# Performance work log

Hardware: AMD Instinct MI355X
Metric: run time of the kernel (lower is better)

Reference implementation:

```python
import jax, jax.numpy as jnp
import numpy as np

N = 100_000           # nodes
E = 3_200_000         # edges (avg degree 32)
DIMS = [64, 80, 160, 112, 160, 176, 96, 144, 96, 128, 96, 160]
NUM_CLASSES = 2


def setup_inputs() -> dict:
    key = jax.random.key(0)
    ks = jax.random.split(key, 64)
    inp = {}
    inp['x'] = jax.random.normal(ks[0], (N, DIMS[0]), dtype=jnp.float32)
    inp['src'] = jax.random.randint(ks[1], (E,), 0, N, dtype=jnp.int32)
    inp['dst'] = jax.random.randint(ks[2], (E,), 0, N, dtype=jnp.int32)
    inp['edata'] = jax.random.uniform(ks[3], (E,), dtype=jnp.float32)
    for i in range(11):
        fi, fo = DIMS[i], DIMS[i + 1]
        inp[f'W{i+1}'] = jax.random.normal(ks[4 + i], (fi, fo), dtype=jnp.float32) / np.float32(np.sqrt(fi))
        inp[f'b{i+1}'] = jnp.zeros((fo,), dtype=jnp.float32)
    inp['Wd1'] = jax.random.normal(ks[20], (160, 140), dtype=jnp.float32) / np.float32(np.sqrt(160))
    inp['bd1'] = jnp.zeros((140,), dtype=jnp.float32)
    inp['Wd2'] = jax.random.normal(ks[21], (140, NUM_CLASSES), dtype=jnp.float32) / np.float32(np.sqrt(140))
    inp['bd2'] = jnp.zeros((NUM_CLASSES,), dtype=jnp.float32)
    inp['mu'] = jnp.asarray(0.0, dtype=jnp.float32)
    inp['sigma'] = jnp.asarray(1.0, dtype=jnp.float32)
    return inp


def _forward(x, src, dst, edata, Ws, bs, Wd1, bd1, Wd2, bd2, mu, sigma):
    n = x.shape[0]
    # edge-weight transform: keep w=1 edges, else gaussian kernel; mu/sigma read via .item() -> stop_gradient
    mu_c = jax.lax.stop_gradient(mu)
    sg_c = jax.lax.stop_gradient(sigma)
    w = jnp.where(edata == 1.0, edata, jnp.exp(-((edata - mu_c) ** 2) / sg_c))  # [E]
    ones_e = jnp.ones_like(edata)
    deg_out = jax.ops.segment_sum(ones_e, src, num_segments=n)  # [N]
    deg_in = jax.ops.segment_sum(ones_e, dst, num_segments=n)   # [N]
    ns = jnp.where(deg_out > 0, jax.lax.rsqrt(jnp.maximum(deg_out, 1.0)), 0.0)
    nd = jnp.where(deg_in > 0, jax.lax.rsqrt(jnp.maximum(deg_in, 1.0)), 0.0)
    coef = ns[src] * w  # [E] src-side norm fused with edge weight

    h = x
    for W, b in zip(Ws, bs):
        m = h[src] * coef[:, None]                               # gather + weight  [E, F]
        agg = jax.ops.segment_sum(m, dst, num_segments=n)        # scatter-add      [N, F]
        h = jax.nn.leaky_relu((agg * nd[:, None]) @ W + b)       # norm + linear + act

    h = jax.nn.leaky_relu(jnp.mean(h, axis=0))                   # mean_nodes -> [160]
    h = jax.nn.leaky_relu(h @ Wd1 + bd1)                         # dropout = identity (eval)
    return jax.nn.sigmoid(h @ Wd2 + bd2)                         # [NUM_CLASSES]


def reference(x, src, dst, edata,
              W1, b1, W2, b2, W3, b3, W4, b4, W5, b5, W6, b6,
              W7, b7, W8, b8, W9, b9, W10, b10, W11, b11,
              Wd1, bd1, Wd2, bd2, mu, sigma):
    Ws = [W1, W2, W3, W4, W5, W6, W7, W8, W9, W10, W11]
    bs = [b1, b2, b3, b4, b5, b6, b7, b8, b9, b10, b11]
    return _forward(x, src, dst, edata, Ws, bs, Wd1, bd1, Wd2, bd2, mu, sigma)
```

## Files before the change

kernel.cpp:

```cpp
#include <hip/hip_runtime.h>

#define LEAKY(v) ((v) > 0.0f ? (v) : 0.01f * (v))
#define SCAN_BLK 1024
#define EPB 4096
#define BKN 256

typedef __bf16 bf16x8 __attribute__((ext_vector_type(8)));
typedef float f32x4 __attribute__((ext_vector_type(4)));

__device__ inline float bflo(unsigned int u) { return __uint_as_float(u << 16); }
__device__ inline float bfhi(unsigned int u) { return __uint_as_float(u & 0xFFFF0000u); }
__device__ inline unsigned int pack2bf(float lo, float hi) {
    unsigned int a = __float_as_uint(lo);
    unsigned int b = __float_as_uint(hi);
    a = (a + 0x7FFFu + ((a >> 16) & 1u)) >> 16;
    b = (b + 0x7FFFu + ((b >> 16) & 1u)) & 0xFFFF0000u;
    return a | b;
}
__device__ inline unsigned short f2bf(float f) {
    unsigned int u = __float_as_uint(f);
    return (unsigned short)((u + 0x7FFFu + ((u >> 16) & 1u)) >> 16);
}

__device__ inline unsigned char f2f8(float v) {
    return (unsigned char)(__builtin_amdgcn_cvt_pk_fp8_f32(v, 0.0f, 0u, false) & 0xFFu);
}


__global__ void histo_kernel(const int* __restrict__ src, const int* __restrict__ dst,
                             int* __restrict__ bh, int E, int NBK, int NBLK, int LEN) {
    extern __shared__ int lds[];
    int* hs = lds;
    int* hd = lds + NBK;
    for (int j = threadIdx.x; j < 2 * NBK; j += 512) lds[j] = 0;
    __syncthreads();
    int b = blockIdx.x;
    int e0 = b * EPB, e1 = min(e0 + EPB, E);
    for (int e = e0 + threadIdx.x; e < e1; e += 512) {
        atomicAdd(&hs[src[e] >> 8], 1);
        atomicAdd(&hd[dst[e] >> 8], 1);
    }
    __syncthreads();
    for (int j = threadIdx.x; j < NBK; j += 512) {
        bh[j * NBLK + b] = hs[j];
        bh[LEN + j * NBLK + b] = hd[j];
    }
}

__global__ void scan1_kernel(const int* __restrict__ deg, int* __restrict__ out,
                             int* __restrict__ bsums, int n) {
    __shared__ int sh[SCAN_BLK];
    int gid = blockIdx.x * SCAN_BLK + threadIdx.x;
    int v = (gid < n) ? deg[gid] : 0;
    sh[threadIdx.x] = v;
    __syncthreads();
    for (int off = 1; off < SCAN_BLK; off <<= 1) {
        int t = (threadIdx.x >= off) ? sh[threadIdx.x - off] : 0;
        __syncthreads();
        sh[threadIdx.x] += t;
        __syncthreads();
    }
    if (gid < n) out[gid + 1] = sh[threadIdx.x];
    if (threadIdx.x == SCAN_BLK - 1) bsums[blockIdx.x] = sh[threadIdx.x];
    if (gid == 0) out[0] = 0;
}

__global__ void scan2_kernel(int* __restrict__ bsums, int nb) {
    __shared__ int sh[SCAN_BLK];
    int v = (threadIdx.x < nb) ? bsums[threadIdx.x] : 0;
    sh[threadIdx.x] = v;
    __syncthreads();
    for (int off = 1; off < SCAN_BLK; off <<= 1) {
        int t = (threadIdx.x >= off) ? sh[threadIdx.x - off] : 0;
        __syncthreads();
        sh[threadIdx.x] += t;
        __syncthreads();
    }
    if (threadIdx.x < nb) bsums[threadIdx.x] = sh[threadIdx.x] - v;
}

__global__ void scan3_kernel(int* __restrict__ out, const int* __restrict__ bsums, int n) {
    int gid = blockIdx.x * SCAN_BLK + threadIdx.x;
    if (gid < n) out[gid + 1] += bsums[blockIdx.x];
}

__global__ void scat_kernel(const int* __restrict__ src, const int* __restrict__ dst,
                            const float* __restrict__ edata,
                            const float* __restrict__ mu, const float* __restrict__ sigma,
                            const int* __restrict__ bhs, unsigned char* __restrict__ srcb8,
                            int2* __restrict__ pay, int E, int NBK, int NBLK, int LEN) {
    extern __shared__ int cur[];
    int* cs = cur;
    int* cd = cur + NBK;
    int b = blockIdx.x;
    for (int j = threadIdx.x; j < NBK; j += 512) {
        cs[j] = bhs[j * NBLK + b];
        cd[j] = bhs[LEN + j * NBLK + b] - E;
    }
    __syncthreads();
    int e0 = b * EPB, e1 = min(e0 + EPB, E);
    for (int e = e0 + threadIdx.x; e < e1; e += 512) {
        int s = src[e];
        int d = dst[e];
        float ed = edata[e];
        float dd = ed - mu[0];
        float w = (ed == 1.0f) ? ed : expf(-(dd * dd) / sigma[0]);
        int ps = atomicAdd(&cs[s >> 8], 1);
        srcb8[ps] = (unsigned char)(s & 255);
        int pd = atomicAdd(&cd[d >> 8], 1);
        pay[pd] = make_int2(s | ((d & 255) << 24), __float_as_int(w));
    }
}

__global__ void ns_kernel(const unsigned char* __restrict__ srcb8, const int* __restrict__ bhs,
                          float* __restrict__ ns, int n, int NBLK) {
    __shared__ int cnt[BKN];
    int b = blockIdx.x;
    int j = threadIdx.x;
    cnt[j] = 0;
    __syncthreads();
    int base = bhs[b * NBLK];
    int endp = bhs[(b + 1) * NBLK];
    for (int e = base + j; e < endp; e += 256)
        atomicAdd(&cnt[srcb8[e]], 1);
    __syncthreads();
    int node = b * BKN + j;
    if (node < n) {
        int c = cnt[j];
        ns[node] = (c > 0) ? rsqrtf((float)c) : 0.0f;
    }
}

__global__ void csr_kernel(const int2* __restrict__ pay, const float* __restrict__ ns,
                           const int* __restrict__ bhs, int* __restrict__ rowptr,
                           float* __restrict__ nd, int2* __restrict__ es,
                           int n, int E, int NBK, int NBLK, int LEN) {
    __shared__ int cnt[BKN];
    __shared__ int cur[BKN];
    int b = blockIdx.x;
    int j = threadIdx.x;
    cnt[j] = 0;
    __syncthreads();
    int base = bhs[LEN + b * NBLK] - E;
    int endp = bhs[LEN + (b + 1) * NBLK] - E;
    for (int e = base + j; e < endp; e += 256)
        atomicAdd(&cnt[(pay[e].x >> 24) & 255], 1);
    __syncthreads();
    int c0 = cnt[j];
    for (int off = 1; off < 256; off <<= 1) {
        int t = (j >= off) ? cnt[j - off] : 0;
        __syncthreads();
        cnt[j] += t;
        __syncthreads();
    }
    int excl = cnt[j] - c0;
    cur[j] = base + excl;
    int node = b * BKN + j;
    if (node < n) {
        rowptr[node] = base + excl;
        nd[node] = (c0 > 0) ? rsqrtf((float)c0) : 0.0f;
    }
    if (b == NBK - 1 && j == 0) rowptr[n] = E;
    __syncthreads();
    for (int e = base + j; e < endp; e += 256) {
        int2 p = pay[e];
        int s = p.x & 0x00FFFFFF;
        float coef = ns[s] * __int_as_float(p.y);
        int pos = atomicAdd(&cur[(p.x >> 24) & 255], 1);
        es[pos] = make_int2(s, __float_as_int(coef));
    }
}


__global__ void x2bf_kernel(const float* __restrict__ x, unsigned short* __restrict__ o16,
                            unsigned char* __restrict__ o8, long long total4) {
    long long i = (long long)blockIdx.x * blockDim.x + threadIdx.x;
    if (i < total4) {
        float4 v = *reinterpret_cast<const float4*>(&x[i * 4]);
        uint2 p;
        p.x = pack2bf(v.x, v.y);
        p.y = pack2bf(v.z, v.w);
        *reinterpret_cast<uint2*>(&o16[i * 4]) = p;
        unsigned int q = __builtin_amdgcn_cvt_pk_fp8_f32(v.x, v.y, 0u, false);
        q = __builtin_amdgcn_cvt_pk_fp8_f32(v.z, v.w, q, true);
        *reinterpret_cast<unsigned int*>(&o8[i * 4]) = q;
    }
}

__global__ void packW_kernel(const float* __restrict__ W, unsigned short* __restrict__ Wp,
                             int FI, int FO) {
    int KB = (FI + 31) / 32;
    int NB = FO / 16;
    int gid = blockIdx.x * blockDim.x + threadIdx.x;
    if (gid >= KB * NB * 64) return;
    int l = gid & 63;
    int tile = gid >> 6;
    int kb = tile % KB;
    int nb = tile / KB;
    int n = nb * 16 + (l & 15);
    int k0 = kb * 32 + (l >> 4) * 8;
    unsigned short tmp[8];
    #pragma unroll
    for (int j = 0; j < 8; ++j) {
        int k = k0 + j;
        tmp[j] = (k < FI) ? f2bf(W[(size_t)k * FO + n]) : (unsigned short)0;
    }
    *reinterpret_cast<uint4*>(&Wp[(size_t)gid * 8]) = *reinterpret_cast<uint4*>(tmp);
}

#define F8ACC16(v, cc) { \
    auto q0 = __builtin_amdgcn_cvt_pk_f32_fp8((v).x, false); \
    auto q1 = __builtin_amdgcn_cvt_pk_f32_fp8((v).x, true);  \
    auto q2 = __builtin_amdgcn_cvt_pk_f32_fp8((v).y, false); \
    auto q3 = __builtin_amdgcn_cvt_pk_f32_fp8((v).y, true);  \
    auto q4 = __builtin_amdgcn_cvt_pk_f32_fp8((v).z, false); \
    auto q5 = __builtin_amdgcn_cvt_pk_f32_fp8((v).z, true);  \
    auto q6 = __builtin_amdgcn_cvt_pk_f32_fp8((v).w, false); \
    auto q7 = __builtin_amdgcn_cvt_pk_f32_fp8((v).w, true);  \
    a[0] = fmaf(q0[0], cc, a[0]);  a[1] = fmaf(q0[1], cc, a[1]); \
    a[2] = fmaf(q1[0], cc, a[2]);  a[3] = fmaf(q1[1], cc, a[3]); \
    a[4] = fmaf(q2[0], cc, a[4]);  a[5] = fmaf(q2[1], cc, a[5]); \
    a[6] = fmaf(q3[0], cc, a[6]);  a[7] = fmaf(q3[1], cc, a[7]); \
    a[8] = fmaf(q4[0], cc, a[8]);  a[9] = fmaf(q4[1], cc, a[9]); \
    a[10] = fmaf(q5[0], cc, a[10]); a[11] = fmaf(q5[1], cc, a[11]); \
    a[12] = fmaf(q6[0], cc, a[12]); a[13] = fmaf(q6[1], cc, a[13]); \
    a[14] = fmaf(q7[0], cc, a[14]); a[15] = fmaf(q7[1], cc, a[15]); }

template<int MODE>
__global__ void agg_kernel(const unsigned char* __restrict__ h8,
                           const int* __restrict__ rowptr, const int2* __restrict__ es,
                           const float* __restrict__ nd, const float* __restrict__ bias,
                           unsigned short* __restrict__ out16, unsigned char* __restrict__ out8,
                           int n, int jt, int ng) {
    int g = threadIdx.x / jt;
    if (g >= ng) return;
    int i = blockIdx.x * ng + g;
    if (i >= n) return;
    int c = (threadIdx.x - g * jt) << 4;
    int F = jt << 4;
    int beg = rowptr[i], end = rowptr[i + 1];
    float a[16] = {};
    int e = beg;
    for (; e + 4 <= end; e += 4) {
        int2 e0 = es[e + 0], e1 = es[e + 1], e2 = es[e + 2], e3 = es[e + 3];
        uint4 v0 = *reinterpret_cast<const uint4*>(&h8[(size_t)e0.x * F + c]);
        uint4 v1 = *reinterpret_cast<const uint4*>(&h8[(size_t)e1.x * F + c]);
        uint4 v2 = *reinterpret_cast<const uint4*>(&h8[(size_t)e2.x * F + c]);
        uint4 v3 = *reinterpret_cast<const uint4*>(&h8[(size_t)e3.x * F + c]);
        float c0 = __int_as_float(e0.y), c1 = __int_as_float(e1.y);
        float c2 = __int_as_float(e2.y), c3 = __int_as_float(e3.y);
        F8ACC16(v0, c0)
        F8ACC16(v1, c1)
        F8ACC16(v2, c2)
        F8ACC16(v3, c3)
    }
    for (; e < end; ++e) {
        int2 e0 = es[e];
        uint4 v0 = *reinterpret_cast<const uint4*>(&h8[(size_t)e0.x * F + c]);
        float c0 = __int_as_float(e0.y);
        F8ACC16(v0, c0)
    }
    if (MODE) {
        float s = nd[i];
        #pragma unroll
        for (int j = 0; j < 16; ++j) {
            float v = a[j] * s + bias[c + j];
            a[j] = LEAKY(v);
        }
    }
    uint4 p0, p1;
    p0.x = pack2bf(a[0], a[1]);   p0.y = pack2bf(a[2], a[3]);
    p0.z = pack2bf(a[4], a[5]);   p0.w = pack2bf(a[6], a[7]);
    p1.x = pack2bf(a[8], a[9]);   p1.y = pack2bf(a[10], a[11]);
    p1.z = pack2bf(a[12], a[13]); p1.w = pack2bf(a[14], a[15]);
    *reinterpret_cast<uint4*>(&out16[(size_t)i * F + c]) = p0;
    *reinterpret_cast<uint4*>(&out16[(size_t)i * F + c + 8]) = p1;
    if (MODE) {
        uint4 q;
        q.x = __builtin_amdgcn_cvt_pk_fp8_f32(a[0], a[1], 0u, false);
        q.x = __builtin_amdgcn_cvt_pk_fp8_f32(a[2], a[3], q.x, true);
        q.y = __builtin_amdgcn_cvt_pk_fp8_f32(a[4], a[5], 0u, false);
        q.y = __builtin_amdgcn_cvt_pk_fp8_f32(a[6], a[7], q.y, true);
        q.z = __builtin_amdgcn_cvt_pk_fp8_f32(a[8], a[9], 0u, false);
        q.z = __builtin_amdgcn_cvt_pk_fp8_f32(a[10], a[11], q.z, true);
        q.w = __builtin_amdgcn_cvt_pk_fp8_f32(a[12], a[13], 0u, false);
        q.w = __builtin_amdgcn_cvt_pk_fp8_f32(a[14], a[15], q.w, true);
        *reinterpret_cast<uint4*>(&out8[(size_t)i * F + c]) = q;
    }
}

template<int FI, int FO, int MODE>
__global__ __launch_bounds__(256) void mm_mfma_kernel(
    const unsigned short* __restrict__ Ab, const float* __restrict__ nd,
    const unsigned short* __restrict__ Wp, const float* __restrict__ bias,
    unsigned short* __restrict__ out16, unsigned char* __restrict__ out8, int n)
{
    constexpr int FIP = (FI + 31) / 32 * 32;
    constexpr int KB = FIP / 32;
    constexpr int NB = FO / 16;
    constexpr int LDA = FIP + 8;
    constexpr int RW = FIP / 8;
    __shared__ unsigned short As[64 * LDA];

    const int t = threadIdx.x;
    const int row0 = blockIdx.x * 64;

    for (int idx = t; idx < 64 * RW; idx += 256) {
        int r = idx / RW;
        int c8 = (idx - r * RW) * 8;
        int grow = row0 + r;
        uint4 v = make_uint4(0u, 0u, 0u, 0u);
        if (grow < n && c8 < FI)
            v = *reinterpret_cast<const uint4*>(&Ab[(size_t)grow * FI + c8]);
        *reinterpret_cast<uint4*>(&As[r * LDA + c8]) = v;
    }
    __syncthreads();

    const int w = t >> 6;
    const int l = t & 63;
    const int arow = (w << 4) + (l & 15);
    const int koff = (l >> 4) << 3;

    bf16x8 a[KB];
    #pragma unroll
    for (int kb = 0; kb < KB; ++kb)
        a[kb] = *reinterpret_cast<const bf16x8*>(&As[arow * LDA + kb * 32 + koff]);

    f32x4 acc[NB] = {};
    #pragma unroll
    for (int nb = 0; nb < NB; ++nb) {
        #pragma unroll
        for (int kb = 0; kb < KB; ++kb) {
            bf16x8 b = *reinterpret_cast<const bf16x8*>(&Wp[(size_t)((nb * KB + kb) * 64 + l) * 8]);
            acc[nb] = __builtin_amdgcn_mfma_f32_16x16x32_bf16(a[kb], b, acc[nb], 0, 0, 0);
        }
    }

    const int col = l & 15;
    const int rb = (l >> 4) << 2;
    #pragma unroll
    for (int r = 0; r < 4; ++r) {
        int grow = row0 + (w << 4) + rb + r;
        if (grow < n) {
            float s = MODE ? nd[grow] : 1.0f;
            #pragma unroll
            for (int nb = 0; nb < NB; ++nb) {
                float v = acc[nb][r];
                if (MODE) {
                    v = v * s + bias[nb * 16 + col];
                    v = LEAKY(v);
                    out16[(size_t)grow * FO + nb * 16 + col] = f2bf(v);
                    out8[(size_t)grow * FO + nb * 16 + col] = f2f8(v);
                } else {
                    out8[(size_t)grow * FO + nb * 16 + col] = f2f8(v);
                }
            }
        }
    }
}

__global__ __launch_bounds__(320) void mean_kernel(const unsigned short* __restrict__ h,
                                                   float* __restrict__ acc, int n) {
    __shared__ float lacc[160];
    int t = threadIdx.x;
    for (int j = t; j < 160; j += 320) lacc[j] = 0.0f;
    __syncthreads();
    int lane = t % 20;
    int rg = t / 20;
    float a0 = 0, a1 = 0, a2 = 0, a3 = 0, a4 = 0, a5 = 0, a6 = 0, a7 = 0;
    for (int i = blockIdx.x * 16 + rg; i < n; i += gridDim.x * 16) {
        uint4 v = *reinterpret_cast<const uint4*>(&h[(size_t)i * 160 + lane * 8]);
        a0 += bflo(v.x); a1 += bfhi(v.x);
        a2 += bflo(v.y); a3 += bfhi(v.y);
        a4 += bflo(v.z); a5 += bfhi(v.z);
        a6 += bflo(v.w); a7 += bfhi(v.w);
    }
    int c = lane * 8;
    atomicAdd(&lacc[c + 0], a0); atomicAdd(&lacc[c + 1], a1);
    atomicAdd(&lacc[c + 2], a2); atomicAdd(&lacc[c + 3], a3);
    atomicAdd(&lacc[c + 4], a4); atomicAdd(&lacc[c + 5], a5);
    atomicAdd(&lacc[c + 6], a6); atomicAdd(&lacc[c + 7], a7);
    __syncthreads();
    for (int j = t; j < 160; j += 320) atomicAdd(&acc[j], lacc[j]);
}

__global__ void head_kernel(const float* __restrict__ acc, const float* __restrict__ Wd1,
                            const float* __restrict__ bd1, const float* __restrict__ Wd2,
                            const float* __restrict__ bd2, float* __restrict__ out, int n) {
    __shared__ float gm[160];
    __shared__ float h1[140];
    int tid = threadIdx.x;
    if (tid < 160) {
        float v = acc[tid] / (float)n;
        gm[tid] = LEAKY(v);
    }
    __syncthreads();
    if (tid < 140) {
        float s = bd1[tid];
        for (int k = 0; k < 160; ++k) s += gm[k] * Wd1[k * 140 + tid];
        h1[tid] = LEAKY(s);
    }
    __syncthreads();
    if (tid < 2) {
        float s = bd2[tid];
        for (int k = 0; k < 140; ++k) s += h1[k] * Wd2[k * 2 + tid];
        out[tid] = 1.0f / (1.0f + expf(-s));
    }
}

extern "C" void kernel_launch(void* const* d_in, const int* in_sizes, int n_in,
                              void* d_out, int out_size, void* d_ws, size_t ws_size,
                              hipStream_t stream) {
    static const int dims[12] = {64, 80, 160, 112, 160, 176, 96, 144, 96, 128, 96, 160};

    const float* x     = (const float*)d_in[0];
    const int*   src   = (const int*)d_in[1];
    const int*   dst   = (const int*)d_in[2];
    const float* edata = (const float*)d_in[3];
    const float* W[11];
    const float* B[11];
    for (int i = 0; i < 11; ++i) {
        W[i] = (const float*)d_in[4 + 2 * i];
        B[i] = (const float*)d_in[5 + 2 * i];
    }
    const float* Wd1   = (const float*)d_in[26];
    const float* bd1   = (const float*)d_in[27];
    const float* Wd2   = (const float*)d_in[28];
    const float* bd2   = (const float*)d_in[29];
    const float* mu    = (const float*)d_in[30];
    const float* sigma = (const float*)d_in[31];
    float* out = (float*)d_out;

    const int N = in_sizes[0] / 64;
    const int E = in_sizes[1];
    const int FMAX = 176;

    const int NBK  = (N + BKN - 1) / BKN;
    const int NBLK = (E + EPB - 1) / EPB;
    const int LEN  = NBK * NBLK;

    size_t woff[11];
    size_t wtot = 0;
    for (int l = 0; l < 11; ++l) {
        woff[l] = wtot;
        int fip = (dims[l] + 31) / 32 * 32;
        wtot += (size_t)fip * dims[l + 1];
    }

    char* wsb = (char*)d_ws;
    size_t o = 0;
    auto alloc = [&](size_t bytes) { void* p = wsb + o; o += (bytes + 255) & ~(size_t)255; return p; };
    unsigned short* hb_main = (unsigned short*)alloc((size_t)N * FMAX * 2);
    unsigned short* hb_t    = (unsigned short*)alloc((size_t)N * FMAX * 2);
    unsigned char*  h8_main = (unsigned char*) alloc((size_t)N * FMAX);
    unsigned char*  h8_t    = (unsigned char*) alloc((size_t)N * FMAX);
    unsigned short* Wp  = (unsigned short*)alloc(wtot * 2);
    int2*  es      = (int2*) alloc((size_t)E * sizeof(int2));
    int2*  pay     = (int2*) alloc((size_t)E * sizeof(int2));
    unsigned char* srcb8 = (unsigned char*)alloc((size_t)E);
    int*   bh      = (int*)  alloc((size_t)(2 * LEN) * sizeof(int));
    int*   bhs     = (int*)  alloc((size_t)(2 * LEN + 1) * sizeof(int));
    int*   rowptr  = (int*)  alloc((size_t)(N + 1) * sizeof(int));
    float* ns      = (float*)alloc((size_t)N * sizeof(float));
    float* nd      = (float*)alloc((size_t)N * sizeof(float));
    int*   bsums   = (int*)  alloc(2048 * sizeof(int));
    float* acc     = (float*)alloc(160 * sizeof(float));

    histo_kernel<<<NBLK, 512, 2 * NBK * sizeof(int), stream>>>(src, dst, bh, E, NBK, NBLK, LEN);
    int snb = (2 * LEN + SCAN_BLK - 1) / SCAN_BLK;
    scan1_kernel<<<snb, SCAN_BLK, 0, stream>>>(bh, bhs, bsums, 2 * LEN);
    scan2_kernel<<<1, SCAN_BLK, 0, stream>>>(bsums, snb);
    scan3_kernel<<<snb, SCAN_BLK, 0, stream>>>(bhs, bsums, 2 * LEN);
    scat_kernel<<<NBLK, 512, 2 * NBK * sizeof(int), stream>>>(src, dst, edata, mu, sigma,
                                                              bhs, srcb8, pay, E, NBK, NBLK, LEN);
    ns_kernel<<<NBK, 256, 0, stream>>>(srcb8, bhs, ns, N, NBLK);
    csr_kernel<<<NBK, 256, 0, stream>>>(pay, ns, bhs, rowptr, nd, es, N, E, NBK, NBLK, LEN);

    long long x4 = (long long)N * 64 / 4;
    x2bf_kernel<<<(int)((x4 + 255) / 256), 256, 0, stream>>>(x, hb_main, h8_main, x4);
    for (int l = 0; l < 11; ++l) {
        int fip = (dims[l] + 31) / 32 * 32;
        int threads = (fip / 32) * (dims[l + 1] / 16) * 64;
        packW_kernel<<<(threads + 255) / 256, 256, 0, stream>>>(W[l], Wp + woff[l],
                                                                dims[l], dims[l + 1]);
    }

    const int mmgrid = (N + 63) / 64;

    #define DO_A(FI, FO, l) { \
        constexpr int jt = FI / 16; constexpr int ng = 256 / jt; \
        agg_kernel<0><<<(N + ng - 1) / ng, 256, 0, stream>>>( \
            h8_main, rowptr, es, nd, B[l], hb_t, nullptr, N, jt, ng); \
        mm_mfma_kernel<FI, FO, 1><<<mmgrid, 256, 0, stream>>>( \
            hb_t, nd, Wp + woff[l], B[l], hb_main, h8_main, N); }

    #define DO_B(FI, FO, l) { \
        mm_mfma_kernel<FI, FO, 0><<<mmgrid, 256, 0, stream>>>( \
            hb_main, nd, Wp + woff[l], B[l], nullptr, h8_t, N); \
        constexpr int jt = FO / 16; constexpr int ng = 256 / jt; \
        agg_kernel<1><<<(N + ng - 1) / ng, 256, 0, stream>>>( \
            h8_t, rowptr, es, nd, B[l], hb_main, h8_main, N, jt, ng); }

    DO_A(64, 80, 0)
    DO_A(80, 160, 1)
    DO_B(160, 112, 2)
    DO_A(112, 160, 3)
    DO_A(160, 176, 4)
    DO_B(176, 96, 5)
    DO_A(96, 144, 6)
    DO_B(144, 96, 7)
    DO_A(96, 128, 8)
    DO_B(128, 96, 9)
    DO_A(96, 160, 10)

    #undef DO_A
    #undef DO_B

    hipMemsetAsync(acc, 0, 160 * sizeof(float), stream);
    mean_kernel<<<256, 320, 0, stream>>>(hb_main, acc, N);
    head_kernel<<<1, 256, 0, stream>>>(acc, Wd1, bd1, Wd2, bd2, out, N);
}
```

Before: 1.346 ms.

## Pad fp8 feature rows to power-of-two stride and skip unused fp8 outputs

```diff
diff --git a/kernel.cpp b/kernel.cpp
--- a/kernel.cpp
+++ b/kernel.cpp
@@ -2,7 +2,7 @@
 
 #define LEAKY(v) ((v) > 0.0f ? (v) : 0.01f * (v))
 #define SCAN_BLK 1024
-#define EPB 4096
+#define EPB 8192
 #define BKN 256
 
 typedef __bf16 bf16x8 __attribute__((ext_vector_type(8)));
@@ -25,6 +25,8 @@
 __device__ inline unsigned char f2f8(float v) {
     return (unsigned char)(__builtin_amdgcn_cvt_pk_fp8_f32(v, 0.0f, 0u, false) & 0xFFu);
 }
+
+constexpr int pad8(int F) { return (F <= 64) ? 64 : (F <= 128 ? 128 : 256); }
 
 
 __global__ void histo_kernel(const int* __restrict__ src, const int* __restrict__ dst,
@@ -172,15 +174,11 @@
 }
 
 
-__global__ void x2bf_kernel(const float* __restrict__ x, unsigned short* __restrict__ o16,
-                            unsigned char* __restrict__ o8, long long total4) {
+__global__ void x2f8_kernel(const float* __restrict__ x, unsigned char* __restrict__ o8,
+                            long long total4) {
     long long i = (long long)blockIdx.x * blockDim.x + threadIdx.x;
     if (i < total4) {
         float4 v = *reinterpret_cast<const float4*>(&x[i * 4]);
-        uint2 p;
-        p.x = pack2bf(v.x, v.y);
-        p.y = pack2bf(v.z, v.w);
-        *reinterpret_cast<uint2*>(&o16[i * 4]) = p;
         unsigned int q = __builtin_amdgcn_cvt_pk_fp8_f32(v.x, v.y, 0u, false);
         q = __builtin_amdgcn_cvt_pk_fp8_f32(v.z, v.w, q, true);
         *reinterpret_cast<unsigned int*>(&o8[i * 4]) = q;
@@ -231,7 +229,7 @@
                            const int* __restrict__ rowptr, const int2* __restrict__ es,
                            const float* __restrict__ nd, const float* __restrict__ bias,
                            unsigned short* __restrict__ out16, unsigned char* __restrict__ out8,
-                           int n, int jt, int ng) {
+                           int n, int jt, int ng, int s8in, int s8out) {
     int g = threadIdx.x / jt;
     if (g >= ng) return;
     int i = blockIdx.x * ng + g;
@@ -243,10 +241,10 @@
     int e = beg;
     for (; e + 4 <= end; e += 4) {
         int2 e0 = es[e + 0], e1 = es[e + 1], e2 = es[e + 2], e3 = es[e + 3];
-        uint4 v0 = *reinterpret_cast<const uint4*>(&h8[(size_t)e0.x * F + c]);
-        uint4 v1 = *reinterpret_cast<const uint4*>(&h8[(size_t)e1.x * F + c]);
-        uint4 v2 = *reinterpret_cast<const uint4*>(&h8[(size_t)e2.x * F + c]);
-        uint4 v3 = *reinterpret_cast<const uint4*>(&h8[(size_t)e3.x * F + c]);
+        uint4 v0 = *reinterpret_cast<const uint4*>(&h8[(size_t)e0.x * s8in + c]);
+        uint4 v1 = *reinterpret_cast<const uint4*>(&h8[(size_t)e1.x * s8in + c]);
+        uint4 v2 = *reinterpret_cast<const uint4*>(&h8[(size_t)e2.x * s8in + c]);
+        uint4 v3 = *reinterpret_cast<const uint4*>(&h8[(size_t)e3.x * s8in + c]);
         float c0 = __int_as_float(e0.y), c1 = __int_as_float(e1.y);
         float c2 = __int_as_float(e2.y), c3 = __int_as_float(e3.y);
         F8ACC16(v0, c0)
@@ -256,7 +254,7 @@
     }
     for (; e < end; ++e) {
         int2 e0 = es[e];
-        uint4 v0 = *reinterpret_cast<const uint4*>(&h8[(size_t)e0.x * F + c]);
+        uint4 v0 = *reinterpret_cast<const uint4*>(&h8[(size_t)e0.x * s8in + c]);
         float c0 = __int_as_float(e0.y);
         F8ACC16(v0, c0)
     }
@@ -285,7 +283,7 @@
         q.z = __builtin_amdgcn_cvt_pk_fp8_f32(a[10], a[11], q.z, true);
         q.w = __builtin_amdgcn_cvt_pk_fp8_f32(a[12], a[13], 0u, false);
         q.w = __builtin_amdgcn_cvt_pk_fp8_f32(a[14], a[15], q.w, true);
-        *reinterpret_cast<uint4*>(&out8[(size_t)i * F + c]) = q;
+        *reinterpret_cast<uint4*>(&out8[(size_t)i * s8out + c]) = q;
     }
 }
 
@@ -293,7 +291,7 @@
 __global__ __launch_bounds__(256) void mm_mfma_kernel(
     const unsigned short* __restrict__ Ab, const float* __restrict__ nd,
     const unsigned short* __restrict__ Wp, const float* __restrict__ bias,
-    unsigned short* __restrict__ out16, unsigned char* __restrict__ out8, int n)
+    unsigned short* __restrict__ out16, unsigned char* __restrict__ out8, int n, int s8)
 {
     constexpr int FIP = (FI + 31) / 32 * 32;
     constexpr int KB = FIP / 32;
@@ -342,17 +340,18 @@
     for (int r = 0; r < 4; ++r) {
         int grow = row0 + (w << 4) + rb + r;
         if (grow < n) {
-            float s = MODE ? nd[grow] : 1.0f;
+            float s = (MODE != 0) ? nd[grow] : 1.0f;
             #pragma unroll
             for (int nb = 0; nb < NB; ++nb) {
                 float v = acc[nb][r];
-                if (MODE) {
+                if (MODE != 0) {
                     v = v * s + bias[nb * 16 + col];
                     v = LEAKY(v);
                     out16[(size_t)grow * FO + nb * 16 + col] = f2bf(v);
-                    out8[(size_t)grow * FO + nb * 16 + col] = f2f8(v);
+                    if (MODE == 1)
+                        out8[(size_t)grow * s8 + nb * 16 + col] = f2f8(v);
                 } else {
-                    out8[(size_t)grow * FO + nb * 16 + col] = f2f8(v);
+                    out8[(size_t)grow * s8 + nb * 16 + col] = f2f8(v);
                 }
             }
         }
@@ -452,8 +451,8 @@
     auto alloc = [&](size_t bytes) { void* p = wsb + o; o += (bytes + 255) & ~(size_t)255; return p; };
     unsigned short* hb_main = (unsigned short*)alloc((size_t)N * FMAX * 2);
     unsigned short* hb_t    = (unsigned short*)alloc((size_t)N * FMAX * 2);
-    unsigned char*  h8_main = (unsigned char*) alloc((size_t)N * FMAX);
-    unsigned char*  h8_t    = (unsigned char*) alloc((size_t)N * FMAX);
+    unsigned char*  h8_main = (unsigned char*) alloc((size_t)N * 256);
+    unsigned char*  h8_t    = (unsigned char*) alloc((size_t)N * 256);
     unsigned short* Wp  = (unsigned short*)alloc(wtot * 2);
     int2*  es      = (int2*) alloc((size_t)E * sizeof(int2));
     int2*  pay     = (int2*) alloc((size_t)E * sizeof(int2));
@@ -477,7 +476,7 @@
     csr_kernel<<<NBK, 256, 0, stream>>>(pay, ns, bhs, rowptr, nd, es, N, E, NBK, NBLK, LEN);
 
     long long x4 = (long long)N * 64 / 4;
-    x2bf_kernel<<<(int)((x4 + 255) / 256), 256, 0, stream>>>(x, hb_main, h8_main, x4);
+    x2f8_kernel<<<(int)((x4 + 255) / 256), 256, 0, stream>>>(x, h8_main, x4);
     for (int l = 0; l < 11; ++l) {
         int fip = (dims[l] + 31) / 32 * 32;
         int threads = (fip / 32) * (dims[l + 1] / 16) * 64;
@@ -487,31 +486,31 @@
 
     const int mmgrid = (N + 63) / 64;
 
-    #define DO_A(FI, FO, l) { \
+    #define DO_A(FI, FO, l, MM)  { \
         constexpr int jt = FI / 16; constexpr int ng = 256 / jt; \
         agg_kernel<0><<<(N + ng - 1) / ng, 256, 0, stream>>>( \
-            h8_main, rowptr, es, nd, B[l], hb_t, nullptr, N, jt, ng); \
-        mm_mfma_kernel<FI, FO, 1><<<mmgrid, 256, 0, stream>>>( \
-            hb_t, nd, Wp + woff[l], B[l], hb_main, h8_main, N); }
+            h8_main, rowptr, es, nd, B[l], hb_t, nullptr, N, jt, ng, pad8(FI), 0); \
+        mm_mfma_kernel<FI, FO, MM><<<mmgrid, 256, 0, stream>>>( \
+            hb_t, nd, Wp + woff[l], B[l], hb_main, h8_main, N, pad8(FO)); }
 
     #define DO_B(FI, FO, l) { \
         mm_mfma_kernel<FI, FO, 0><<<mmgrid, 256, 0, stream>>>( \
-            hb_main, nd, Wp + woff[l], B[l], nullptr, h8_t, N); \
+            hb_main, nd, Wp + woff[l], B[l], nullptr, h8_t, N, pad8(FO)); \
         constexpr int jt = FO / 16; constexpr int ng = 256 / jt; \
         agg_kernel<1><<<(N + ng - 1) / ng, 256, 0, stream>>>( \
-            h8_t, rowptr, es, nd, B[l], hb_main, h8_main, N, jt, ng); }
-
-    DO_A(64, 80, 0)
-    DO_A(80, 160, 1)
+            h8_t, rowptr, es, nd, B[l], hb_main, h8_main, N, jt, ng, pad8(FO), pad8(FO)); }
+
+    DO_A(64, 80, 0, 1)
+    DO_A(80, 160, 1, 2)
     DO_B(160, 112, 2)
-    DO_A(112, 160, 3)
-    DO_A(160, 176, 4)
+    DO_A(112, 160, 3, 1)
+    DO_A(160, 176, 4, 2)
     DO_B(176, 96, 5)
-    DO_A(96, 144, 6)
+    DO_A(96, 144, 6, 2)
     DO_B(144, 96, 7)
-    DO_A(96, 128, 8)
+    DO_A(96, 128, 8, 2)
     DO_B(128, 96, 9)
-    DO_A(96, 160, 10)
+    DO_A(96, 160, 10, 2)
 
     #undef DO_A
     #undef DO_B
```

After: 1.199 ms. 1.12x faster.
